# Kernel optimization log

Hardware: AMD Instinct MI355X
Metric: run time of the kernel (lower is better)

The kernel has to match this reference:

```python
import jax, jax.numpy as jnp
import numpy as np

D_MODEL = 1024
NUM_HEADS = 16
D_K = D_MODEL // NUM_HEADS
THETA = 10000.0
SEQ_LEN = 4096


def setup_inputs() -> dict:
    key = jax.random.key(0)
    ks = jax.random.split(key, 5)
    std = (2.0 / (D_MODEL + D_MODEL)) ** 0.5
    x = jax.random.normal(ks[0], (1, SEQ_LEN, D_MODEL), dtype=jnp.float32)
    Wq = jax.random.normal(ks[1], (D_MODEL, D_MODEL), dtype=jnp.float32) * std
    Wk = jax.random.normal(ks[2], (D_MODEL, D_MODEL), dtype=jnp.float32) * std
    Wv = jax.random.normal(ks[3], (D_MODEL, D_MODEL), dtype=jnp.float32) * std
    Wo = jax.random.normal(ks[4], (D_MODEL, D_MODEL), dtype=jnp.float32) * std
    return {"x": x, "Wq": Wq, "Wk": Wk, "Wv": Wv, "Wo": Wo}


def _rope(x, cos, sin):
    # x: [B, H, S, d_k]; cos/sin: [S, d_k//2] broadcast over B,H
    x_even = x[..., ::2]
    x_odd = x[..., 1::2]
    r_even = x_even * cos - x_odd * sin
    r_odd = x_even * sin + x_odd * cos
    # re-interleave: stack on last axis then flatten pairs
    return jnp.stack([r_even, r_odd], axis=-1).reshape(x.shape)


def _forward(x, Wq, Wk, Wv, Wo):
    B, S, _ = x.shape
    # projections (weight stored [out, in])
    q = jnp.einsum('bsd,od->bso', x, Wq)
    k = jnp.einsum('bsd,od->bso', x, Wk)
    v = jnp.einsum('bsd,od->bso', x, Wv)
    # split heads -> [B, H, S, d_k]
    q = q.reshape(B, S, NUM_HEADS, D_K).transpose(0, 2, 1, 3)
    k = k.reshape(B, S, NUM_HEADS, D_K).transpose(0, 2, 1, 3)
    v = v.reshape(B, S, NUM_HEADS, D_K).transpose(0, 2, 1, 3)
    # RoPE tables
    freqs_d = 1.0 / (THETA ** (jnp.arange(0, D_K, 2, dtype=jnp.float32) / D_K))
    pos = jnp.arange(S, dtype=jnp.float32)
    freqs = pos[:, None] * freqs_d[None, :]  # [S, d_k//2]
    cos, sin = jnp.cos(freqs), jnp.sin(freqs)
    q = _rope(q, cos, sin)
    k = _rope(k, cos, sin)
    # scaled dot-product attention with causal mask
    scores = jnp.einsum('bhqd,bhkd->bhqk', q, k) / (D_K ** 0.5)
    causal = jnp.tril(jnp.ones((S, S), dtype=bool))
    scores = jnp.where(causal, scores, -jnp.inf)
    weights = jax.nn.softmax(scores, axis=-1)
    out = jnp.einsum('bhqk,bhkd->bhqd', weights, v)
    out = out.transpose(0, 2, 1, 3).reshape(B, S, D_MODEL)
    return jnp.einsum('bsd,od->bso', out, Wo)


def reference(x, Wq, Wk, Wv, Wo):
    return _forward(x, Wq, Wk, Wv, Wo)
```

## Files before the change

### kernel.cpp

```cpp
#include <hip/hip_runtime.h>
#include <math.h>

#define SEQ 4096
#define DMODEL 1024
#define NHEAD 16
#define DKH 64

typedef __attribute__((ext_vector_type(8))) short bf16x8;
typedef __attribute__((ext_vector_type(4))) float f32x4;

__device__ __forceinline__ ushort f2b(float x) {
    unsigned u = __float_as_uint(x);
    return (ushort)((u + 0x7fffu + ((u >> 16) & 1u)) >> 16);
}
__device__ __forceinline__ float b2f(ushort u) {
    return __uint_as_float(((unsigned)u) << 16);
}

#define DPP_ROR_F(x, ctrl) \
    __int_as_float(__builtin_amdgcn_update_dpp(__float_as_int(x), __float_as_int(x), (ctrl), 0xf, 0xf, false))

__device__ __forceinline__ float rowmax16(float x) {
    x = fmaxf(x, DPP_ROR_F(x, 0x121));
    x = fmaxf(x, DPP_ROR_F(x, 0x122));
    x = fmaxf(x, DPP_ROR_F(x, 0x124));
    x = fmaxf(x, DPP_ROR_F(x, 0x128));
    return x;
}
__device__ __forceinline__ float rowsum16(float x) {
    x += DPP_ROR_F(x, 0x121);
    x += DPP_ROR_F(x, 0x122);
    x += DPP_ROR_F(x, 0x124);
    x += DPP_ROR_F(x, 0x128);
    return x;
}

__global__ __launch_bounds__(256)
void conv_bf16(const float* __restrict__ x,  const float* __restrict__ wq,
               const float* __restrict__ wk, const float* __restrict__ wv,
               const float* __restrict__ wo,
               ushort* __restrict__ xb,  ushort* __restrict__ wqb,
               ushort* __restrict__ wkb, ushort* __restrict__ wvb,
               ushort* __restrict__ wob) {
    const int b = blockIdx.x;
    const float* src; ushort* dst; int idx;
    if (b < 4096) {
        src = x; dst = xb; idx = b * 256 + threadIdx.x;
    } else {
        int t = b - 4096;
        int which = t >> 10;
        idx = (t & 1023) * 256 + threadIdx.x;
        if      (which == 0) { src = wq; dst = wqb; }
        else if (which == 1) { src = wk; dst = wkb; }
        else if (which == 2) { src = wv; dst = wvb; }
        else                 { src = wo; dst = wob; }
    }
    float4 f = ((const float4*)src)[idx];
    ushort4 o;
    o.x = f2b(f.x); o.y = f2b(f.y); o.z = f2b(f.z); o.w = f2b(f.w);
    ((ushort4*)dst)[idx] = o;
}

#define GSTR 40

template<bool OUT_BF16>
__global__ __launch_bounds__(256)
void gemm_bf16(const ushort* __restrict__ A, const ushort* __restrict__ B,
               void* __restrict__ Cv, int M, int N, int K) {
    __shared__ __attribute__((aligned(16))) ushort As[128 * GSTR];
    __shared__ __attribute__((aligned(16))) ushort Bs[128 * GSTR];

    const int tid  = threadIdx.x;
    const int lane = tid & 63;
    const int w    = tid >> 6;
    const int wr   = w >> 1, wc = w & 1;
    const int lrow = lane & 15, lgrp = lane >> 4;
    const int m0 = blockIdx.y * 128;
    const int n0 = blockIdx.x * 128;

    const int srow = tid >> 2;
    const int skc  = (tid & 3) * 8;
    const ushort* Ap0 = A + (size_t)(m0 + srow) * K + skc;
    const ushort* Ap1 = Ap0 + (size_t)64 * K;
    const ushort* Bp0 = B + (size_t)(n0 + srow) * K + skc;
    const ushort* Bp1 = Bp0 + (size_t)64 * K;
    ushort* sA0 = &As[srow * GSTR + skc];
    ushort* sA1 = &As[(srow + 64) * GSTR + skc];
    ushort* sB0 = &Bs[srow * GSTR + skc];
    ushort* sB1 = &Bs[(srow + 64) * GSTR + skc];

    f32x4 acc[4][4];
#pragma unroll
    for (int i = 0; i < 4; i++)
#pragma unroll
        for (int j = 0; j < 4; j++) acc[i][j] = (f32x4){0.f, 0.f, 0.f, 0.f};

    bf16x8 ra0 = *(const bf16x8*)(Ap0);
    bf16x8 ra1 = *(const bf16x8*)(Ap1);
    bf16x8 rb0 = *(const bf16x8*)(Bp0);
    bf16x8 rb1 = *(const bf16x8*)(Bp1);

    const int NT = K >> 5;
    for (int kt = 0; kt < NT; kt++) {
        __syncthreads();
        *(bf16x8*)sA0 = ra0;  *(bf16x8*)sA1 = ra1;
        *(bf16x8*)sB0 = rb0;  *(bf16x8*)sB1 = rb1;
        __syncthreads();

        if (kt + 1 < NT) {
            const int ko = (kt + 1) * 32;
            ra0 = *(const bf16x8*)(Ap0 + ko);
            ra1 = *(const bf16x8*)(Ap1 + ko);
            rb0 = *(const bf16x8*)(Bp0 + ko);
            rb1 = *(const bf16x8*)(Bp1 + ko);
        }

        bf16x8 af[4], bfr[4];
#pragma unroll
        for (int i = 0; i < 4; i++)
            af[i] = *(const bf16x8*)&As[(wr * 64 + i * 16 + lrow) * GSTR + lgrp * 8];
#pragma unroll
        for (int j = 0; j < 4; j++)
            bfr[j] = *(const bf16x8*)&Bs[(wc * 64 + j * 16 + lrow) * GSTR + lgrp * 8];
#pragma unroll
        for (int i = 0; i < 4; i++)
#pragma unroll
            for (int j = 0; j < 4; j++)
                acc[i][j] = __builtin_amdgcn_mfma_f32_16x16x32_bf16(af[i], bfr[j], acc[i][j], 0, 0, 0);
    }

#pragma unroll
    for (int i = 0; i < 4; i++) {
#pragma unroll
        for (int j = 0; j < 4; j++) {
#pragma unroll
            for (int r = 0; r < 4; r++) {
                const size_t row = m0 + wr * 64 + i * 16 + lgrp * 4 + r;
                const size_t col = n0 + wc * 64 + j * 16 + lrow;
                if constexpr (OUT_BF16)
                    ((ushort*)Cv)[row * N + col] = f2b(acc[i][j][r]);
                else
                    ((float*)Cv)[row * N + col] = acc[i][j][r];
            }
        }
    }
}

__global__ __launch_bounds__(256)
void rope_bf16(ushort* __restrict__ q, ushort* __restrict__ k) {
    int idx = blockIdx.x * 256 + threadIdx.x;
    if (idx >= SEQ * (DMODEL / 2)) return;
    int s  = idx >> 9;
    int j  = idx & 511;
    int hh = j >> 5;
    int i  = j & 31;
    const float LOG1E4_OVER32 = 0.28782313662425572f;
    float freq = __expf(-(float)i * LOG1E4_OVER32);
    float ang  = (float)s * freq;
    float c, sn;
    __sincosf(ang, &sn, &c);
    size_t base = (size_t)s * DMODEL + hh * DKH + 2 * i;
    float e = b2f(q[base]), o_ = b2f(q[base + 1]);
    q[base]     = f2b(e * c - o_ * sn);
    q[base + 1] = f2b(e * sn + o_ * c);
    e = b2f(k[base]); o_ = b2f(k[base + 1]);
    k[base]     = f2b(e * c - o_ * sn);
    k[base + 1] = f2b(e * sn + o_ * c);
}

#define LSTR 72

__global__ __launch_bounds__(256)
void attn_mfma(const ushort* __restrict__ Q, const ushort* __restrict__ K,
               const ushort* __restrict__ V, ushort* __restrict__ O) {
    __shared__ __attribute__((aligned(16))) ushort Ks[64 * LSTR];
    __shared__ __attribute__((aligned(16))) ushort Vs[64 * LSTR];
    __shared__ __attribute__((aligned(16))) ushort Ps[4][16 * LSTR];

    const int tid  = threadIdx.x;
    const int w    = tid >> 6;
    const int lane = tid & 63;
    const int lrow = lane & 15;
    const int lgrp = lane >> 4;
    const int h    = blockIdx.y;
    const int qi   = (int)gridDim.x - 1 - (int)blockIdx.x;
    const int qbase = qi * 64;

    const int qr = qbase + w * 16 + lrow;
    const ushort* qp = Q + (size_t)qr * DMODEL + h * DKH + lgrp * 8;
    bf16x8 qfrag[2];
    qfrag[0] = *(const bf16x8*)(qp);
    qfrag[1] = *(const bf16x8*)(qp + 32);

    f32x4 o_acc[4];
#pragma unroll
    for (int t = 0; t < 4; t++) o_acc[t] = (f32x4){0.f, 0.f, 0.f, 0.f};
    float m_r[4], l_r[4];
#pragma unroll
    for (int r = 0; r < 4; r++) { m_r[r] = -INFINITY; l_r[r] = 0.f; }

    const int row0 = tid >> 3;
    const int col0 = (tid & 7) * 8;
    const ushort* Kp = K + (size_t)h * DKH;
    const ushort* Vp = V + (size_t)h * DKH;

    const int ktmax = qi;
    bf16x8 rk[2], rv[2];
#pragma unroll
    for (int cc = 0; cc < 2; cc++) {
        const int row = row0 + cc * 32;
        rk[cc] = *(const bf16x8*)(Kp + (size_t)row * DMODEL + col0);
        rv[cc] = *(const bf16x8*)(Vp + (size_t)row * DMODEL + col0);
    }

    for (int kt = 0; kt <= ktmax; kt++) {
        const int kbase = kt * 64;
        __syncthreads();
#pragma unroll
        for (int cc = 0; cc < 2; cc++) {
            const int row = row0 + cc * 32;
            *(bf16x8*)&Ks[row * LSTR + col0] = rk[cc];
            const int vrow = row ^ (col0 & 56);
#pragma unroll
            for (int jj = 0; jj < 8; jj++)
                Vs[(col0 + jj) * LSTR + vrow] = (ushort)rv[cc][jj];
        }
        __syncthreads();

        if (kt < ktmax) {
            const size_t nb = (size_t)(kbase + 64) * DMODEL;
#pragma unroll
            for (int cc = 0; cc < 2; cc++) {
                const int row = row0 + cc * 32;
                rk[cc] = *(const bf16x8*)(Kp + nb + (size_t)row * DMODEL + col0);
                rv[cc] = *(const bf16x8*)(Vp + nb + (size_t)row * DMODEL + col0);
            }
        }

        f32x4 s[4];
#pragma unroll
        for (int n = 0; n < 4; n++) {
            f32x4 acc = (f32x4){0.f, 0.f, 0.f, 0.f};
#pragma unroll
            for (int ks = 0; ks < 2; ks++) {
                bf16x8 kf = *(const bf16x8*)&Ks[(n * 16 + lrow) * LSTR + lgrp * 8 + ks * 32];
                acc = __builtin_amdgcn_mfma_f32_16x16x32_bf16(qfrag[ks], kf, acc, 0, 0, 0);
            }
            s[n] = acc;
        }

        const int myq = qbase + w * 16 + lgrp * 4;
#pragma unroll
        for (int n = 0; n < 4; n++) {
            const int key = kbase + n * 16 + lrow;
#pragma unroll
            for (int r = 0; r < 4; r++)
                s[n][r] = (key > myq + r) ? -INFINITY : s[n][r] * 0.125f;
        }

        float alpha[4];
#pragma unroll
        for (int r = 0; r < 4; r++) {
            float t0 = fmaxf(fmaxf(s[0][r], s[1][r]), fmaxf(s[2][r], s[3][r]));
            float mnew = fmaxf(m_r[r], rowmax16(t0));
            alpha[r] = __expf(m_r[r] - mnew);
            m_r[r] = mnew;
        }
#pragma unroll
        for (int t = 0; t < 4; t++)
#pragma unroll
            for (int r = 0; r < 4; r++) o_acc[t][r] *= alpha[r];

        float psum[4] = {0.f, 0.f, 0.f, 0.f};
#pragma unroll
        for (int n = 0; n < 4; n++) {
#pragma unroll
            for (int r = 0; r < 4; r++) {
                float p = __expf(s[n][r] - m_r[r]);
                psum[r] += p;
                Ps[w][(lgrp * 4 + r) * LSTR + n * 16 + lrow] = f2b(p);
            }
        }
#pragma unroll
        for (int r = 0; r < 4; r++)
            l_r[r] = l_r[r] * alpha[r] + rowsum16(psum[r]);

#pragma unroll
        for (int ks = 0; ks < 2; ks++) {
            bf16x8 pa = *(const bf16x8*)&Ps[w][lrow * LSTR + lgrp * 8 + ks * 32];
#pragma unroll
            for (int t = 0; t < 4; t++) {
                const int xr = (2 * t + (lrow >> 3)) << 3;
                bf16x8 vb = *(const bf16x8*)&Vs[(t * 16 + lrow) * LSTR + ((lgrp * 8 + ks * 32) ^ xr)];
                o_acc[t] = __builtin_amdgcn_mfma_f32_16x16x32_bf16(pa, vb, o_acc[t], 0, 0, 0);
            }
        }
    }

    float invl[4];
#pragma unroll
    for (int r = 0; r < 4; r++) invl[r] = 1.0f / l_r[r];
    ushort* op = O + (size_t)(qbase + w * 16) * DMODEL + h * DKH;
#pragma unroll
    for (int t = 0; t < 4; t++)
#pragma unroll
        for (int r = 0; r < 4; r++)
            op[(size_t)(lgrp * 4 + r) * DMODEL + t * 16 + lrow] = f2b(o_acc[t][r] * invl[r]);
}

extern "C" void kernel_launch(void* const* d_in, const int* in_sizes, int n_in,
                              void* d_out, int out_size, void* d_ws, size_t ws_size,
                              hipStream_t stream) {
    const float* x  = (const float*)d_in[0];
    const float* Wq = (const float*)d_in[1];
    const float* Wk = (const float*)d_in[2];
    const float* Wv = (const float*)d_in[3];
    const float* Wo = (const float*)d_in[4];
    float* out = (float*)d_out;

    const size_t NM = (size_t)SEQ * DMODEL;
    const size_t NW = (size_t)DMODEL * DMODEL;
    ushort* qb  = (ushort*)d_ws;
    ushort* kb  = qb + NM;
    ushort* vb  = kb + NM;
    ushort* ob  = vb + NM;
    ushort* xb  = ob + NM;
    ushort* wqb = xb + NM;
    ushort* wkb = wqb + NW;
    ushort* wvb = wkb + NW;
    ushort* wob = wvb + NW;

    conv_bf16<<<8192, 256, 0, stream>>>(x, Wq, Wk, Wv, Wo, xb, wqb, wkb, wvb, wob);

    dim3 ggrid(DMODEL / 128, SEQ / 128);
    gemm_bf16<true><<<ggrid, 256, 0, stream>>>(xb, wqb, qb, SEQ, DMODEL, DMODEL);
    gemm_bf16<true><<<ggrid, 256, 0, stream>>>(xb, wkb, kb, SEQ, DMODEL, DMODEL);
    gemm_bf16<true><<<ggrid, 256, 0, stream>>>(xb, wvb, vb, SEQ, DMODEL, DMODEL);

    rope_bf16<<<SEQ * (DMODEL / 2) / 256, 256, 0, stream>>>(qb, kb);

    attn_mfma<<<dim3(SEQ / 64, NHEAD), 256, 0, stream>>>(qb, kb, vb, ob);

    gemm_bf16<false><<<ggrid, 256, 0, stream>>>(ob, wob, out, SEQ, DMODEL, DMODEL);
}
```

Baseline: 367.4 us.

## Split attention key tiles across two wave groups with LDS merge of partial softmax

The attention block grows to 512 threads. Two groups of four waves each take alternating 64-key tiles for the same 64 query rows, and their partial outputs and softmax statistics (m, l) are merged through shared memory at the end. This gives more parallel work per block on the long causal rows, paid for with extra LDS, a final combine step and idle group-1 work on the odd tile count. It also switches to exp2 with a pre-scaled log2e factor, skips the rescale when no row max grew, and raises wave priority around the MFMA sections.

Result: slower. 387.6 us (+5.5%).

```diff
diff --git a/kernel.cpp b/kernel.cpp
--- a/kernel.cpp
+++ b/kernel.cpp
@@ -169,16 +169,19 @@
 }
 
 #define LSTR 72
-
-__global__ __launch_bounds__(256)
+#define SCALE2 0.18033688011112042f
+
+__global__ __launch_bounds__(512)
 void attn_mfma(const ushort* __restrict__ Q, const ushort* __restrict__ K,
                const ushort* __restrict__ V, ushort* __restrict__ O) {
-    __shared__ __attribute__((aligned(16))) ushort Ks[64 * LSTR];
-    __shared__ __attribute__((aligned(16))) ushort Vs[64 * LSTR];
-    __shared__ __attribute__((aligned(16))) ushort Ps[4][16 * LSTR];
+    __shared__ __attribute__((aligned(16))) ushort Ks[2][64 * LSTR];
+    __shared__ __attribute__((aligned(16))) ushort Vs[2][64 * LSTR];
+    __shared__ __attribute__((aligned(16))) ushort Ps[8][16 * LSTR];
 
     const int tid  = threadIdx.x;
     const int w    = tid >> 6;
+    const int g    = w >> 2;
+    const int wg   = w & 3;
     const int lane = tid & 63;
     const int lrow = lane & 15;
     const int lgrp = lane >> 4;
@@ -186,7 +189,7 @@
     const int qi   = (int)gridDim.x - 1 - (int)blockIdx.x;
     const int qbase = qi * 64;
 
-    const int qr = qbase + w * 16 + lrow;
+    const int qr = qbase + wg * 16 + lrow;
     const ushort* qp = Q + (size_t)qr * DMODEL + h * DKH + lgrp * 8;
     bf16x8 qfrag[2];
     qfrag[0] = *(const bf16x8*)(qp);
@@ -199,36 +202,51 @@
 #pragma unroll
     for (int r = 0; r < 4; r++) { m_r[r] = -INFINITY; l_r[r] = 0.f; }
 
-    const int row0 = tid >> 3;
-    const int col0 = (tid & 7) * 8;
+    const int tg   = tid & 255;
+    const int row0 = tg >> 3;
+    const int col0 = (tg & 7) * 8;
     const ushort* Kp = K + (size_t)h * DKH;
     const ushort* Vp = V + (size_t)h * DKH;
 
     const int ktmax = qi;
+    const int nIter = (ktmax + 2) >> 1;
+
     bf16x8 rk[2], rv[2];
-#pragma unroll
-    for (int cc = 0; cc < 2; cc++) {
-        const int row = row0 + cc * 32;
-        rk[cc] = *(const bf16x8*)(Kp + (size_t)row * DMODEL + col0);
-        rv[cc] = *(const bf16x8*)(Vp + (size_t)row * DMODEL + col0);
-    }
-
-    for (int kt = 0; kt <= ktmax; kt++) {
-        const int kbase = kt * 64;
-        __syncthreads();
+    {
+        const int kt0 = (g <= ktmax) ? g : ktmax;
+        const size_t nb = (size_t)kt0 * 64 * DMODEL;
 #pragma unroll
         for (int cc = 0; cc < 2; cc++) {
             const int row = row0 + cc * 32;
-            *(bf16x8*)&Ks[row * LSTR + col0] = rk[cc];
-            const int vrow = row ^ (col0 & 56);
-#pragma unroll
-            for (int jj = 0; jj < 8; jj++)
-                Vs[(col0 + jj) * LSTR + vrow] = (ushort)rv[cc][jj];
-        }
+            rk[cc] = *(const bf16x8*)(Kp + nb + (size_t)row * DMODEL + col0);
+            rv[cc] = *(const bf16x8*)(Vp + nb + (size_t)row * DMODEL + col0);
+        }
+    }
+
+    for (int it = 0; it < nIter; it++) {
+        const int kt = 2 * it + g;
+        const bool active = (kt <= ktmax);
+        const int kbase = kt * 64;
+
         __syncthreads();
-
-        if (kt < ktmax) {
-            const size_t nb = (size_t)(kbase + 64) * DMODEL;
+        if (active) {
+#pragma unroll
+            for (int cc = 0; cc < 2; cc++) {
+                const int row = row0 + cc * 32;
+                *(bf16x8*)&Ks[g][row * LSTR + col0] = rk[cc];
+                const int vrow = row ^ (col0 & 56);
+#pragma unroll
+                for (int jj = 0; jj < 8; jj++)
+                    Vs[g][(col0 + jj) * LSTR + vrow] = (ushort)rv[cc][jj];
+            }
+        }
+        __syncthreads();
+
+        if (!active) continue;
+
+        {
+            const int ktn = (kt + 2 <= ktmax) ? kt + 2 : ktmax;
+            const size_t nb = (size_t)ktn * 64 * DMODEL;
 #pragma unroll
             for (int cc = 0; cc < 2; cc++) {
                 const int row = row0 + cc * 32;
@@ -238,74 +256,112 @@
         }
 
         f32x4 s[4];
+        __builtin_amdgcn_s_setprio(1);
 #pragma unroll
         for (int n = 0; n < 4; n++) {
             f32x4 acc = (f32x4){0.f, 0.f, 0.f, 0.f};
 #pragma unroll
             for (int ks = 0; ks < 2; ks++) {
-                bf16x8 kf = *(const bf16x8*)&Ks[(n * 16 + lrow) * LSTR + lgrp * 8 + ks * 32];
+                bf16x8 kf = *(const bf16x8*)&Ks[g][(n * 16 + lrow) * LSTR + lgrp * 8 + ks * 32];
                 acc = __builtin_amdgcn_mfma_f32_16x16x32_bf16(qfrag[ks], kf, acc, 0, 0, 0);
             }
             s[n] = acc;
         }
-
-        const int myq = qbase + w * 16 + lgrp * 4;
+        __builtin_amdgcn_s_setprio(0);
+
+        const int myq = qbase + wg * 16 + lgrp * 4;
 #pragma unroll
         for (int n = 0; n < 4; n++) {
             const int key = kbase + n * 16 + lrow;
 #pragma unroll
             for (int r = 0; r < 4; r++)
-                s[n][r] = (key > myq + r) ? -INFINITY : s[n][r] * 0.125f;
-        }
-
-        float alpha[4];
+                s[n][r] = (key > myq + r) ? -INFINITY : s[n][r] * SCALE2;
+        }
+
+        float rmax[4];
 #pragma unroll
         for (int r = 0; r < 4; r++) {
             float t0 = fmaxf(fmaxf(s[0][r], s[1][r]), fmaxf(s[2][r], s[3][r]));
-            float mnew = fmaxf(m_r[r], rowmax16(t0));
-            alpha[r] = __expf(m_r[r] - mnew);
-            m_r[r] = mnew;
-        }
-#pragma unroll
-        for (int t = 0; t < 4; t++)
-#pragma unroll
-            for (int r = 0; r < 4; r++) o_acc[t][r] *= alpha[r];
+            rmax[r] = rowmax16(t0);
+        }
+        bool grew = false;
+#pragma unroll
+        for (int r = 0; r < 4; r++) grew = grew || (rmax[r] > m_r[r]);
+        if (__any((int)grew)) {
+#pragma unroll
+            for (int r = 0; r < 4; r++) {
+                float mnew = fmaxf(m_r[r], rmax[r]);
+                float al = exp2f(m_r[r] - mnew);
+                m_r[r] = mnew;
+                l_r[r] *= al;
+#pragma unroll
+                for (int t = 0; t < 4; t++) o_acc[t][r] *= al;
+            }
+        }
 
         float psum[4] = {0.f, 0.f, 0.f, 0.f};
 #pragma unroll
         for (int n = 0; n < 4; n++) {
 #pragma unroll
             for (int r = 0; r < 4; r++) {
-                float p = __expf(s[n][r] - m_r[r]);
+                float p = exp2f(s[n][r] - m_r[r]);
                 psum[r] += p;
                 Ps[w][(lgrp * 4 + r) * LSTR + n * 16 + lrow] = f2b(p);
             }
         }
 #pragma unroll
         for (int r = 0; r < 4; r++)
-            l_r[r] = l_r[r] * alpha[r] + rowsum16(psum[r]);
-
+            l_r[r] += rowsum16(psum[r]);
+
+        __builtin_amdgcn_s_setprio(1);
 #pragma unroll
         for (int ks = 0; ks < 2; ks++) {
             bf16x8 pa = *(const bf16x8*)&Ps[w][lrow * LSTR + lgrp * 8 + ks * 32];
 #pragma unroll
             for (int t = 0; t < 4; t++) {
                 const int xr = (2 * t + (lrow >> 3)) << 3;
-                bf16x8 vb = *(const bf16x8*)&Vs[(t * 16 + lrow) * LSTR + ((lgrp * 8 + ks * 32) ^ xr)];
+                bf16x8 vb = *(const bf16x8*)&Vs[g][(t * 16 + lrow) * LSTR + ((lgrp * 8 + ks * 32) ^ xr)];
                 o_acc[t] = __builtin_amdgcn_mfma_f32_16x16x32_bf16(pa, vb, o_acc[t], 0, 0, 0);
             }
         }
-    }
-
-    float invl[4];
-#pragma unroll
-    for (int r = 0; r < 4; r++) invl[r] = 1.0f / l_r[r];
-    ushort* op = O + (size_t)(qbase + w * 16) * DMODEL + h * DKH;
-#pragma unroll
-    for (int t = 0; t < 4; t++)
-#pragma unroll
-        for (int r = 0; r < 4; r++)
-            op[(size_t)(lgrp * 4 + r) * DMODEL + t * 16 + lrow] = f2b(o_acc[t][r] * invl[r]);
+        __builtin_amdgcn_s_setprio(0);
+    }
+
+    float* abuf  = (float*)&Ks[0][0];
+    float* mlbuf = (float*)&Vs[0][0];
+    __syncthreads();
+    if (g == 1) {
+        float* a  = abuf  + ((size_t)wg * 64 + lane) * 16;
+        float* ml = mlbuf + ((size_t)wg * 64 + lane) * 8;
+#pragma unroll
+        for (int t = 0; t < 4; t++)
+#pragma unroll
+            for (int r = 0; r < 4; r++) a[t * 4 + r] = o_acc[t][r];
+#pragma unroll
+        for (int r = 0; r < 4; r++) { ml[r] = m_r[r]; ml[4 + r] = l_r[r]; }
+    }
+    __syncthreads();
+    if (g == 0) {
+        const float* a  = abuf  + ((size_t)wg * 64 + lane) * 16;
+        const float* ml = mlbuf + ((size_t)wg * 64 + lane) * 8;
+        float e0[4], e1[4], invl[4];
+#pragma unroll
+        for (int r = 0; r < 4; r++) {
+            float m1 = ml[r], l1 = ml[4 + r];
+            float ms = fmaxf(m_r[r], m1);
+            e0[r] = exp2f(m_r[r] - ms);
+            e1[r] = exp2f(m1 - ms);
+            invl[r] = 1.0f / (l_r[r] * e0[r] + l1 * e1[r]);
+        }
+        ushort* op = O + (size_t)(qbase + wg * 16) * DMODEL + h * DKH;
+#pragma unroll
+        for (int t = 0; t < 4; t++)
+#pragma unroll
+            for (int r = 0; r < 4; r++) {
+                float v = (o_acc[t][r] * e0[r] + a[t * 4 + r] * e1[r]) * invl[r];
+                op[(size_t)(lgrp * 4 + r) * DMODEL + t * 16 + lrow] = f2b(v);
+            }
+    }
 }
 
 extern "C" void kernel_launch(void* const* d_in, const int* in_sizes, int n_in,
@@ -339,7 +395,7 @@
 
     rope_bf16<<<SEQ * (DMODEL / 2) / 256, 256, 0, stream>>>(qb, kb);
 
-    attn_mfma<<<dim3(SEQ / 64, NHEAD), 256, 0, stream>>>(qb, kb, vb, ob);
+    attn_mfma<<<dim3(SEQ / 64, NHEAD), 512, 0, stream>>>(qb, kb, vb, ob);
 
     gemm_bf16<false><<<ggrid, 256, 0, stream>>>(ob, wob, out, SEQ, DMODEL, DMODEL);
 }
```
